# Kernel tuning notes

Hardware: AMD Instinct MI355X
Metric: run time of the kernel (lower is better)

## Reference

```python
import jax, jax.numpy as jnp
import numpy as np

N_ANCHORS = 262144
B = 4
G = 64
IM_SIZE = 1024.0
STRADDLE = 0.0
POS_THR = 0.5
NEG_THR = 0.3
FG_FRAC = 0.3
SAMPLE_BATCH = 512
TARGET_FG = int(FG_FRAC * SAMPLE_BATCH)  # 153
NEG_LOGIT = -1e9


def _jaccard(a, b):
    # Detectron-legacy '+1' box convention. a:[N,4], b:[G,4] -> [N,G]
    area_a = (a[:, 2] - a[:, 0] + 1.0) * (a[:, 3] - a[:, 1] + 1.0)
    area_b = (b[:, 2] - b[:, 0] + 1.0) * (b[:, 3] - b[:, 1] + 1.0)
    lt = jnp.maximum(a[:, None, :2], b[None, :, :2])
    rb = jnp.minimum(a[:, None, 2:], b[None, :, 2:])
    wh = jnp.clip(rb - lt + 1.0, 0.0)
    inter = wh[..., 0] * wh[..., 1]
    return inter / (area_a[:, None] + area_b[None, :] - inter)


def _bbox_transform_inv(ex, gt):
    ew = ex[:, 2] - ex[:, 0] + 1.0
    eh = ex[:, 3] - ex[:, 1] + 1.0
    ecx = ex[:, 0] + 0.5 * ew
    ecy = ex[:, 1] + 0.5 * eh
    gw = gt[:, 2] - gt[:, 0] + 1.0
    gh = gt[:, 3] - gt[:, 1] + 1.0
    gcx = gt[:, 0] + 0.5 * gw
    gcy = gt[:, 1] + 0.5 * gh
    return jnp.stack([(gcx - ecx) / ew, (gcy - ecy) / eh,
                      jnp.log(gw / ew), jnp.log(gh / eh)], axis=1)


def _match_single(boxes, gt_boxes, gt_ignore, im_info, key):
    # mask-based (jit-friendly) equivalent of forward_single_image; outside
    # anchors keep label -1 / targets 0, which reproduces the unmap() step.
    n = boxes.shape[0]
    im_h, im_w = im_info[0], im_info[1]
    inside = ((boxes[:, 0] >= -STRADDLE) & (boxes[:, 1] >= -STRADDLE)
              & (boxes[:, 2] < im_w + STRADDLE + 1.0)
              & (boxes[:, 3] < im_h + STRADDLE + 1.0))
    valid_gt = gt_ignore == 0  # gt_boxes[gt_ignore_labels == 0]
    iou = jnp.where(inside[:, None] & valid_gt[None, :], _jaccard(boxes, gt_boxes), 0.0)
    a2g_max = iou.max(axis=1)
    a2g_idx = iou.argmax(axis=1)
    g2a_max = iou.max(axis=0)
    g2a_max = jnp.where(g2a_max == 0.0, 1.0, g2a_max)  # avoid matching all-zero cols
    with_max = (iou == g2a_max[None, :]).any(axis=1)   # ensure_closest_box
    pos = inside & (with_max | (a2g_max >= POS_THR))
    labels = jnp.where(pos, 1, -1).astype(jnp.int32)
    # subsample positives down to TARGET_FG by random priority (keeps exactly
    # min(fg_num, TARGET_FG) positives, like the permutation-based disable)
    kp, kn = jax.random.split(key)
    prio = jnp.where(pos, jax.random.uniform(kp, (n,)), -jnp.inf)
    rank = jnp.argsort(jnp.argsort(-prio))
    labels = jnp.where(pos & (rank >= TARGET_FG), -1, labels)
    # sample negatives with replacement (torch.multinomial(..., replacement=True))
    num_fg = (labels > 0).sum()
    target_bg = SAMPLE_BATCH - num_fg
    neg = inside & (a2g_max < NEG_THR)
    do_sample = neg.sum() > target_bg
    samp = jax.random.categorical(kn, jnp.where(neg, 0.0, NEG_LOGIT), shape=(SAMPLE_BATCH,))
    valid_s = jnp.arange(SAMPLE_BATCH) < target_bg
    idx = jnp.where(valid_s, samp, n)  # invalid samples write to padded slot
    lab_ext = jnp.concatenate([labels, jnp.full((1,), -1, jnp.int32)])
    lab_samp = lab_ext.at[idx].set(0)[:n]
    labels = jnp.where(do_sample, lab_samp, labels)
    pos_final = labels > 0
    deltas = _bbox_transform_inv(boxes, gt_boxes[a2g_idx])
    bbox_targets = jnp.where(pos_final[:, None], deltas, 0.0)
    return labels, bbox_targets


def setup_inputs() -> dict:
    key = jax.random.key(0)
    k1, k2, k3, k4, k5, k6 = jax.random.split(key, 6)
    axy = jax.random.uniform(k1, (N_ANCHORS, 2), minval=-50.0, maxval=950.0)
    awh = jax.random.uniform(k2, (N_ANCHORS, 2), minval=16.0, maxval=160.0)
    boxes = jnp.concatenate([axy, axy + awh], axis=1)
    gxy = jax.random.uniform(k3, (B, G, 2), minval=0.0, maxval=800.0)
    gwh = jax.random.uniform(k4, (B, G, 2), minval=32.0, maxval=220.0)
    gt_boxes = jnp.concatenate([gxy, gxy + gwh], axis=2)
    gt_labels = jax.random.randint(k5, (B, G), 0, 80)
    gt_ignore_labels = jax.random.randint(k6, (B, G), 0, 2)
    im_info = jnp.tile(jnp.array([IM_SIZE, IM_SIZE, 1.0], jnp.float32), (B, 1))
    return {"boxes": boxes, "gt_boxes": gt_boxes, "gt_labels": gt_labels,
            "gt_ignore_labels": gt_ignore_labels, "im_info": im_info}


def reference(boxes, gt_boxes, gt_labels, gt_ignore_labels, im_info):
    # gt_labels is accepted but unused, exactly as in the torch module
    keys = jax.random.split(jax.random.key(42), gt_boxes.shape[0])
    labels, bbox_targets = jax.vmap(_match_single, in_axes=(None, 0, 0, 0, 0))(
        boxes.reshape(-1, 4), gt_boxes, gt_ignore_labels, im_info, keys)
    return labels, bbox_targets
```

## Files before the change

### kernel.cpp

```cpp
#include <hip/hip_runtime.h>
#include <stdint.h>

#define NANCH   262144
#define NB      4
#define NG      64
#define TGT_FG  153
#define SB      512
#define IDXMASK 262143u
#define NSH     8
#define SHCAP   (NANCH/NSH)

#define WS_PCNT     0
#define WS_KTH      4096
#define WS_TBG      4160
#define WS_DOSAMP   4224
#define WS_NUMPOS   4288
#define WS_G2A      4352
#define WS_SAMPKEY  8192
#define WS_ZERO_BYTES 24576
#define WS_GMAXC    32768
#define WS_A2G      294912
#define WS_NEG      (WS_A2G + NB*NANCH)
#define WS_POS      (WS_NEG + NB*NANCH*4)

#define PCNT_AT(pcnt, b, sh, L) ((pcnt)[(((b) * NSH + (sh)) * 2 + (L)) * 16])

struct RngKeys { uint32_t kp[NB][2]; uint32_t kn[NB][2]; };

#define TFR(r) { x0 += x1; x1 = (x1 << (r)) | (x1 >> (32 - (r))); x1 ^= x0; }
__host__ __device__ inline void tf2x32(uint32_t k0, uint32_t k1,
                                       uint32_t x0, uint32_t x1,
                                       uint32_t &o0, uint32_t &o1) {
  uint32_t k2 = k0 ^ k1 ^ 0x1BD11BDAu;
  x0 += k0; x1 += k1;
  TFR(13) TFR(15) TFR(26) TFR(6)   x0 += k1; x1 += k2 + 1u;
  TFR(17) TFR(29) TFR(16) TFR(24)  x0 += k2; x1 += k0 + 2u;
  TFR(13) TFR(15) TFR(26) TFR(6)   x0 += k0; x1 += k1 + 3u;
  TFR(17) TFR(29) TFR(16) TFR(24)  x0 += k1; x1 += k2 + 4u;
  TFR(13) TFR(15) TFR(26) TFR(6)   x0 += k2; x1 += k0 + 5u;
  o0 = x0; o1 = x1;
}

__host__ __device__ inline void tf_ctr(uint32_t k0, uint32_t k1, uint32_t i,
                                       uint32_t &o0, uint32_t &o1) {
  tf2x32(k0, k1, 0u, i, o0, o1);
}

__device__ __forceinline__ uint32_t draw_bits(uint32_t k0, uint32_t k1,
                                              uint32_t idx) {
  uint32_t o0, o1;
  tf_ctr(k0, k1, idx, o0, o1);
  return o0 ^ o1;
}

#define ROTL1(x, r) __builtin_amdgcn_alignbit((x), (x), 32 - (r))
#define TFQ(r) { x0 += x1; x1 = ROTL1(x1, r); x1 ^= x0; }
__device__ __forceinline__ uint32_t tf_bits_fast(uint32_t k0, uint32_t k1,
                                                 uint32_t k2, uint32_t x0,
                                                 uint32_t x1) {
  TFQ(13) TFQ(15) TFQ(26) TFQ(6)   x0 += k1; x1 += k2 + 1u;
  TFQ(17) TFQ(29) TFQ(16) TFQ(24)  x0 += k2; x1 += k0 + 2u;
  TFQ(13) TFQ(15) TFQ(26) TFQ(6)   x0 += k0; x1 += k1 + 3u;
  TFQ(17) TFQ(29) TFQ(16) TFQ(24)  x0 += k1; x1 += k2 + 4u;
  TFQ(13) TFQ(15) TFQ(26) TFQ(6)   x0 += k2; x1 += k0 + 5u;
  return x0 ^ x1;
}

__device__ __forceinline__ float box_area(float x1, float y1, float x2, float y2) {
#pragma clang fp contract(off)
  return ((x2 - x1) + 1.0f) * ((y2 - y1) + 1.0f);
}

__device__ __forceinline__ float iou_pair(float ax1, float ay1, float ax2, float ay2,
                                          float areaA, float gx1, float gy1,
                                          float gx2, float gy2, float areaB) {
#pragma clang fp contract(off)
  float ltx = fmaxf(ax1, gx1), lty = fmaxf(ay1, gy1);
  float rbx = fminf(ax2, gx2), rby = fminf(ay2, gy2);
  float w = fmaxf((rbx - ltx) + 1.0f, 0.0f);
  float h = fmaxf((rby - lty) + 1.0f, 0.0f);
  float inter = w * h;
  return inter / ((areaA + areaB) - inter);
}

__global__ __launch_bounds__(256) void k_g2amax(
    const float4* __restrict__ boxes, const float4* __restrict__ gtb,
    const int* __restrict__ gti, const float* __restrict__ iminfo,
    float* __restrict__ gmaxc) {
  int bx = blockIdx.x;
  int b = bx >> 8, chunk = bx & 255;
  int t = threadIdx.x, j = t & 63, sub = t >> 6;
  float4 g = gtb[b * NG + j];
  bool valid = (gti[b * NG + j] == 0);
  float areaB = box_area(g.x, g.y, g.z, g.w);
  float thrx = iminfo[b * 3 + 1] + 1.0f;
  float thry = iminfo[b * 3 + 0] + 1.0f;
  float m = 0.0f;
  int base = chunk * 1024 + sub * 256;
  #pragma unroll 2
  for (int i = 0; i < 256; ++i) {
    float4 bb = boxes[base + i];
    bool inside = (bb.x >= -0.0f) && (bb.y >= -0.0f) && (bb.z < thrx) && (bb.w < thry);
    float areaA = box_area(bb.x, bb.y, bb.z, bb.w);
    float v = iou_pair(bb.x, bb.y, bb.z, bb.w, areaA, g.x, g.y, g.z, g.w, areaB);
    v = (inside && valid) ? v : 0.0f;
    m = fmaxf(m, v);
  }
  __shared__ float red[4][64];
  red[sub][j] = m;
  __syncthreads();
  if (t < 64) {
    float mm = fmaxf(fmaxf(red[0][t], red[1][t]), fmaxf(red[2][t], red[3][t]));
    gmaxc[((b << 8) + chunk) * 64 + t] = mm;
  }
}

__global__ __launch_bounds__(256) void k_g2afin(
    const float* __restrict__ gmaxc, float* __restrict__ g2a) {
  int b = blockIdx.x, t = threadIdx.x;
  int j = t & 63, part = t >> 6;
  float m = 0.0f;
  for (int c = part * 64; c < part * 64 + 64; ++c)
    m = fmaxf(m, gmaxc[((b << 8) + c) * 64 + j]);
  __shared__ float red[4][64];
  red[part][j] = m;
  __syncthreads();
  if (t < 64)
    g2a[b * NG + t] = fmaxf(fmaxf(red[0][t], red[1][t]),
                            fmaxf(red[2][t], red[3][t]));
}

__global__ __launch_bounds__(256) void k_label(
    const float4* __restrict__ boxes, const float4* __restrict__ gtb,
    const int* __restrict__ gti, const float* __restrict__ iminfo,
    const float* __restrict__ g2a, float* __restrict__ labels,
    unsigned char* __restrict__ a2g, unsigned long long* __restrict__ pos_keys,
    unsigned int* __restrict__ neg_list, int* __restrict__ pcnt, RngKeys rk) {
  int bx = blockIdx.x;
  int b = bx >> 10, blk = bx & 1023;
  int t = threadIdx.x;
  int sh = blk & (NSH - 1);
  __shared__ float4 sg[NG];
  __shared__ float sab[NG], sval[NG], sadj[NG];
  if (t < NG) {
    float4 g = gtb[b * NG + t];
    sg[t] = g;
    sab[t] = box_area(g.x, g.y, g.z, g.w);
    sval[t] = (gti[b * NG + t] == 0) ? 1.0f : 0.0f;
    float gm = g2a[b * NG + t];
    sadj[t] = (gm == 0.0f) ? 1.0f : gm;
  }
  __syncthreads();
  int a = blk * 256 + t;
  float4 bb = boxes[a];
  float thrx = iminfo[b * 3 + 1] + 1.0f, thry = iminfo[b * 3 + 0] + 1.0f;
  bool inside = (bb.x >= -0.0f) && (bb.y >= -0.0f) && (bb.z < thrx) && (bb.w < thry);
  float areaA = box_area(bb.x, bb.y, bb.z, bb.w);
  float maxv = 0.0f; int amax = 0; bool wm = false;
  #pragma unroll 8
  for (int j = 0; j < NG; ++j) {
    float4 g = sg[j];
    float v = iou_pair(bb.x, bb.y, bb.z, bb.w, areaA, g.x, g.y, g.z, g.w, sab[j]);
    v = (inside && (sval[j] != 0.0f)) ? v : 0.0f;
    wm = wm || (v == sadj[j]);
    if (v > maxv) { maxv = v; amax = j; }
  }
  bool pos = inside && (wm || (maxv >= 0.5f));
  bool neg = inside && (maxv < 0.3f);
  labels[b * NANCH + a] = pos ? 1.0f : -1.0f;
  a2g[b * NANCH + a] = (unsigned char)amax;
  unsigned long long mpos = __ballot(pos);
  unsigned long long mneg = __ballot(neg);
  int lane = t & 63, wid = t >> 6;
  __shared__ int wc[4][2];
  __shared__ int bbase[2];
  if (lane == 0) { wc[wid][0] = __popcll(mpos); wc[wid][1] = __popcll(mneg); }
  __syncthreads();
  if (t == 0) {
    bbase[0] = atomicAdd(&PCNT_AT(pcnt, b, sh, 0),
                         wc[0][0] + wc[1][0] + wc[2][0] + wc[3][0]);
    bbase[1] = atomicAdd(&PCNT_AT(pcnt, b, sh, 1),
                         wc[0][1] + wc[1][1] + wc[2][1] + wc[3][1]);
  }
  __syncthreads();
  unsigned long long lt = (1ull << lane) - 1ull;
  if (pos) {
    int off = bbase[0] + __popcll(mpos & lt);
    for (int w = 0; w < wid; ++w) off += wc[w][0];
    uint32_t bits = draw_bits(rk.kp[b][0], rk.kp[b][1], (uint32_t)a);
    unsigned long long key =
        (((unsigned long long)(bits >> 9)) << 18) | (unsigned long long)(IDXMASK - (uint32_t)a);
    pos_keys[(size_t)b * NANCH + (size_t)sh * SHCAP + off] = key;
  }
  if (neg) {
    int off = bbase[1] + __popcll(mneg & lt);
    for (int w = 0; w < wid; ++w) off += wc[w][1];
    neg_list[(size_t)b * NANCH + (size_t)sh * SHCAP + off] = (unsigned int)a;
  }
}

__global__ __launch_bounds__(256) void k_catsel(
    const unsigned int* __restrict__ neg_list,
    const unsigned long long* __restrict__ pos_keys,
    const int* __restrict__ pcnt, unsigned long long* __restrict__ samp_key,
    unsigned long long* __restrict__ kth, int* __restrict__ tbg,
    int* __restrict__ dosamp, int* __restrict__ numpos, RngKeys rk) {
  int bx = blockIdx.x;
  int t = threadIdx.x, lane = t & 63, wid = t >> 6;

  if (bx < NB) {
    int b = bx;
    __shared__ int cw[4];
    int scnt[NSH]; int np = 0, nnb = 0;
    #pragma unroll
    for (int sh = 0; sh < NSH; ++sh) {
      scnt[sh] = PCNT_AT(pcnt, b, sh, 0);
      np += scnt[sh];
      nnb += PCNT_AT(pcnt, b, sh, 1);
    }
    int nf = np < TGT_FG ? np : TGT_FG;
    int targ = SB - nf;
    if (t == 0) { tbg[b] = targ; dosamp[b] = (nnb > targ) ? 1 : 0; numpos[b] = np; }
    if (np <= TGT_FG) { if (t == 0) kth[b] = 0ull; return; }
    unsigned long long pref = 0ull;
    int r = TGT_FG;
    for (int bit = 40; bit >= 0; --bit) {
      unsigned long long cand = pref | (1ull << bit);
      unsigned long long mask = ~((1ull << bit) - 1ull);
      int c = 0;
      for (int sh = 0; sh < NSH; ++sh) {
        const unsigned long long* keys =
            pos_keys + (size_t)b * NANCH + (size_t)sh * SHCAP;
        for (int i = t; i < scnt[sh]; i += 256)
          c += ((keys[i] & mask) == cand) ? 1 : 0;
      }
      #pragma unroll
      for (int off = 32; off; off >>= 1) c += __shfl_xor(c, off, 64);
      __syncthreads();
      if (lane == 0) cw[wid] = c;
      __syncthreads();
      int total = cw[0] + cw[1] + cw[2] + cw[3];
      if (total >= r) pref = cand; else r -= total;
    }
    if (t == 0) kth[b] = pref;
    return;
  }

  int bx2 = bx - NB;
  int sh = bx2 & (NSH - 1);
  int pr = (bx2 >> 3) & 255;
  int b  = bx2 >> 11;
  int np = 0;
  #pragma unroll
  for (int s = 0; s < NSH; ++s) np += PCNT_AT(pcnt, b, s, 0);
  int targ = SB - (np < TGT_FG ? np : TGT_FG);
  int s0 = pr * 2;
  if (s0 >= targ) return;
  int nn = PCNT_AT(pcnt, b, sh, 1);
  uint32_t k0 = rk.kn[b][0], k1 = rk.kn[b][1];
  uint32_t k2 = k0 ^ k1 ^ 0x1BD11BDAu;
  uint32_t xb0 = ((uint32_t)s0 << 18) + k1;
  uint32_t xb1 = ((uint32_t)(s0 + 1) << 18) + k1;
  unsigned long long b0 = 0ull, b1 = 0ull;
  const unsigned int* nl = neg_list + (size_t)b * NANCH + (size_t)sh * SHCAP;
#define PROC1(A) { uint32_t a_ = (A); \
    unsigned long long inv64 = (unsigned long long)(IDXMASK - a_); \
    { uint32_t bits = tf_bits_fast(k0, k1, k2, k0, xb0 + a_); \
      unsigned long long key = (((unsigned long long)(bits >> 9)) << 18) | inv64; \
      if (key > b0) b0 = key; } \
    { uint32_t bits = tf_bits_fast(k0, k1, k2, k0, xb1 + a_); \
      unsigned long long key = (((unsigned long long)(bits >> 9)) << 18) | inv64; \
      if (key > b1) b1 = key; } }
  int nv = nn >> 2;
  const uint4* nl4 = (const uint4*)nl;
  for (int iv = t; iv < nv; iv += 256) {
    uint4 q = nl4[iv];
    PROC1(q.x) PROC1(q.y) PROC1(q.z) PROC1(q.w)
  }
  for (int i = (nv << 2) + t; i < nn; i += 256) { PROC1(nl[i]) }
#undef PROC1
  #pragma unroll
  for (int off = 32; off; off >>= 1) {
    unsigned long long o0 = __shfl_xor(b0, off, 64); if (o0 > b0) b0 = o0;
    unsigned long long o1 = __shfl_xor(b1, off, 64); if (o1 > b1) b1 = o1;
  }
  __shared__ unsigned long long red[4][2];
  if (lane == 0) { red[wid][0] = b0; red[wid][1] = b1; }
  __syncthreads();
  if (t < 2) {
    int j = t;
    unsigned long long m = red[0][j];
    if (red[1][j] > m) m = red[1][j];
    if (red[2][j] > m) m = red[2][j];
    if (red[3][j] > m) m = red[3][j];
    if (s0 + j < targ) atomicMax(&samp_key[b * SB + s0 + j], m);
  }
}

__global__ __launch_bounds__(256) void k_disable(
    const unsigned long long* __restrict__ pos_keys, const int* __restrict__ pcnt,
    const int* __restrict__ numpos, const unsigned long long* __restrict__ kth,
    float* __restrict__ labels) {
  int b = blockIdx.x >> 6, blk = blockIdx.x & 63;
  if (numpos[b] <= TGT_FG) return;
  int sh = blk & (NSH - 1), sub = blk >> 3;
  int cnt = PCNT_AT(pcnt, b, sh, 0);
  unsigned long long K = kth[b];
  const unsigned long long* keys = pos_keys + (size_t)b * NANCH + (size_t)sh * SHCAP;
  for (int i = sub * 256 + threadIdx.x; i < cnt; i += 8 * 256) {
    unsigned long long key = keys[i];
    if (key < K) {
      int a = (int)(IDXMASK - (uint32_t)(key & (unsigned long long)IDXMASK));
      labels[b * NANCH + a] = -1.0f;
    }
  }
}

__global__ __launch_bounds__(256) void k_scatter(
    const unsigned long long* __restrict__ samp_key, const int* __restrict__ tbg,
    const int* __restrict__ dosamp, float* __restrict__ labels) {
  int b = blockIdx.x >> 1;
  int s = ((blockIdx.x & 1) << 8) | threadIdx.x;
  if (!dosamp[b]) return;
  if (s < tbg[b]) {
    unsigned long long key = samp_key[b * SB + s];
    int a = (int)(IDXMASK - (uint32_t)(key & (unsigned long long)IDXMASK));
    labels[b * NANCH + a] = 0.0f;
  }
}

__global__ __launch_bounds__(256) void k_targets(
    const float4* __restrict__ boxes, const float4* __restrict__ gtb,
    const unsigned char* __restrict__ a2g, const float* __restrict__ labels,
    float4* __restrict__ tout) {
  int bx = blockIdx.x;
  int b = bx >> 10, blk = bx & 1023;
  int a = blk * 256 + threadIdx.x;
  float lab = labels[b * NANCH + a];
  float4 o = make_float4(0.f, 0.f, 0.f, 0.f);
  if (lab > 0.0f) {
    float4 e = boxes[a];
    float4 g = gtb[b * NG + a2g[b * NANCH + a]];
    float ew = e.z - e.x + 1.0f, eh = e.w - e.y + 1.0f;
    float ecx = e.x + 0.5f * ew, ecy = e.y + 0.5f * eh;
    float gw = g.z - g.x + 1.0f, gh = g.w - g.y + 1.0f;
    float gcx = g.x + 0.5f * gw, gcy = g.y + 0.5f * gh;
    o.x = (gcx - ecx) / ew;
    o.y = (gcy - ecy) / eh;
    o.z = logf(gw / ew);
    o.w = logf(gh / eh);
  }
  tout[(size_t)b * NANCH + a] = o;
}

extern "C" void kernel_launch(void* const* d_in, const int* in_sizes, int n_in,
                              void* d_out, int out_size, void* d_ws, size_t ws_size,
                              hipStream_t stream) {
  const float4* boxes  = (const float4*)d_in[0];
  const float4* gtb    = (const float4*)d_in[1];
  const int*    gti    = (const int*)d_in[3];
  const float*  iminfo = (const float*)d_in[4];
  float*  labels = (float*)d_out;
  float4* tout   = (float4*)(labels + (size_t)NB * NANCH);

  char* wsb = (char*)d_ws;
  int*                pcnt     = (int*)(wsb + WS_PCNT);
  unsigned long long* kth      = (unsigned long long*)(wsb + WS_KTH);
  int*                tbg      = (int*)(wsb + WS_TBG);
  int*                dosamp   = (int*)(wsb + WS_DOSAMP);
  int*                numpos   = (int*)(wsb + WS_NUMPOS);
  float*              g2a_f    = (float*)(wsb + WS_G2A);
  unsigned long long* samp_key = (unsigned long long*)(wsb + WS_SAMPKEY);
  float*              gmaxc    = (float*)(wsb + WS_GMAXC);
  unsigned char*      a2g      = (unsigned char*)(wsb + WS_A2G);
  unsigned int*       neg_list = (unsigned int*)(wsb + WS_NEG);
  unsigned long long* pos_keys = (unsigned long long*)(wsb + WS_POS);

  RngKeys rk;
  for (int b = 0; b < NB; ++b) {
    uint32_t a0, a1;
    tf_ctr(0u, 42u, (uint32_t)b, a0, a1);
    tf_ctr(a0, a1, 0u, rk.kp[b][0], rk.kp[b][1]);
    tf_ctr(a0, a1, 1u, rk.kn[b][0], rk.kn[b][1]);
  }

  hipMemsetAsync(wsb, 0, WS_ZERO_BYTES, stream);
  k_g2amax <<<NB * (NANCH / 1024), 256, 0, stream>>>(boxes, gtb, gti, iminfo, gmaxc);
  k_g2afin <<<NB, 256, 0, stream>>>(gmaxc, g2a_f);
  k_label  <<<NB * (NANCH / 256), 256, 0, stream>>>(boxes, gtb, gti, iminfo, g2a_f,
                                                    labels, a2g, pos_keys, neg_list,
                                                    pcnt, rk);
  k_catsel <<<NB + NB * 256 * NSH, 256, 0, stream>>>(neg_list, pos_keys, pcnt,
                                                     samp_key, kth, tbg, dosamp,
                                                     numpos, rk);
  k_disable<<<NB * 64, 256, 0, stream>>>(pos_keys, pcnt, numpos, kth, labels);
  k_scatter<<<NB * 2, 256, 0, stream>>>(samp_key, tbg, dosamp, labels);
  k_targets<<<NB * (NANCH / 256), 256, 0, stream>>>(boxes, gtb, a2g, labels, tout);
}
```

Measured before the change: 745.7 us.

## Fuse memset, g2a finalize and positive-disable into neighbouring kernels

Drops the workspace memset by having block 0 of k_g2amax zero it. Drops k_g2afin by having every k_label block redo the per-GT max reduction over the chunk maxima. Drops k_disable by having k_targets recompute each positive's random key and compare it against the k-th threshold. The aim is to remove three launches and their dependency gaps. The cost is that every one of the 4096 k_label blocks now reads the full 64 KB gmaxc slice for its batch, which adds heavy redundant L2 traffic, and k_targets does extra Threefry work for positive anchors.

```diff
diff --git a/kernel.cpp b/kernel.cpp
--- a/kernel.cpp
+++ b/kernel.cpp
@@ -14,10 +14,8 @@
 #define WS_KTH      4096
 #define WS_TBG      4160
 #define WS_DOSAMP   4224
-#define WS_NUMPOS   4288
-#define WS_G2A      4352
 #define WS_SAMPKEY  8192
-#define WS_ZERO_BYTES 24576
+#define WS_ZERO_WORDS 6144
 #define WS_GMAXC    32768
 #define WS_A2G      294912
 #define WS_NEG      (WS_A2G + NB*NANCH)
@@ -86,10 +84,15 @@
 __global__ __launch_bounds__(256) void k_g2amax(
     const float4* __restrict__ boxes, const float4* __restrict__ gtb,
     const int* __restrict__ gti, const float* __restrict__ iminfo,
-    float* __restrict__ gmaxc) {
+    float* __restrict__ gmaxc, unsigned int* __restrict__ wszero) {
   int bx = blockIdx.x;
+  int t = threadIdx.x;
+  if (bx == 0) {
+    #pragma unroll
+    for (int i = t; i < WS_ZERO_WORDS; i += 256) wszero[i] = 0u;
+  }
   int b = bx >> 8, chunk = bx & 255;
-  int t = threadIdx.x, j = t & 63, sub = t >> 6;
+  int j = t & 63, sub = t >> 6;
   float4 g = gtb[b * NG + j];
   bool valid = (gti[b * NG + j] == 0);
   float areaB = box_area(g.x, g.y, g.z, g.w);
@@ -115,25 +118,10 @@
   }
 }
 
-__global__ __launch_bounds__(256) void k_g2afin(
-    const float* __restrict__ gmaxc, float* __restrict__ g2a) {
-  int b = blockIdx.x, t = threadIdx.x;
-  int j = t & 63, part = t >> 6;
-  float m = 0.0f;
-  for (int c = part * 64; c < part * 64 + 64; ++c)
-    m = fmaxf(m, gmaxc[((b << 8) + c) * 64 + j]);
-  __shared__ float red[4][64];
-  red[part][j] = m;
-  __syncthreads();
-  if (t < 64)
-    g2a[b * NG + t] = fmaxf(fmaxf(red[0][t], red[1][t]),
-                            fmaxf(red[2][t], red[3][t]));
-}
-
 __global__ __launch_bounds__(256) void k_label(
     const float4* __restrict__ boxes, const float4* __restrict__ gtb,
     const int* __restrict__ gti, const float* __restrict__ iminfo,
-    const float* __restrict__ g2a, float* __restrict__ labels,
+    const float* __restrict__ gmaxc, float* __restrict__ labels,
     unsigned char* __restrict__ a2g, unsigned long long* __restrict__ pos_keys,
     unsigned int* __restrict__ neg_list, int* __restrict__ pcnt, RngKeys rk) {
   int bx = blockIdx.x;
@@ -142,12 +130,23 @@
   int sh = blk & (NSH - 1);
   __shared__ float4 sg[NG];
   __shared__ float sab[NG], sval[NG], sadj[NG];
+  __shared__ float red2[4][64];
+  {
+    int j = t & 63, part = t >> 6;
+    float m = 0.0f;
+    for (int c = part * 64; c < part * 64 + 64; ++c)
+      m = fmaxf(m, gmaxc[((b << 8) + c) * 64 + j]);
+    red2[part][j] = m;
+  }
   if (t < NG) {
     float4 g = gtb[b * NG + t];
     sg[t] = g;
     sab[t] = box_area(g.x, g.y, g.z, g.w);
     sval[t] = (gti[b * NG + t] == 0) ? 1.0f : 0.0f;
-    float gm = g2a[b * NG + t];
+  }
+  __syncthreads();
+  if (t < 64) {
+    float gm = fmaxf(fmaxf(red2[0][t], red2[1][t]), fmaxf(red2[2][t], red2[3][t]));
     sadj[t] = (gm == 0.0f) ? 1.0f : gm;
   }
   __syncthreads();
@@ -204,7 +203,7 @@
     const unsigned long long* __restrict__ pos_keys,
     const int* __restrict__ pcnt, unsigned long long* __restrict__ samp_key,
     unsigned long long* __restrict__ kth, int* __restrict__ tbg,
-    int* __restrict__ dosamp, int* __restrict__ numpos, RngKeys rk) {
+    int* __restrict__ dosamp, RngKeys rk) {
   int bx = blockIdx.x;
   int t = threadIdx.x, lane = t & 63, wid = t >> 6;
 
@@ -220,7 +219,7 @@
     }
     int nf = np < TGT_FG ? np : TGT_FG;
     int targ = SB - nf;
-    if (t == 0) { tbg[b] = targ; dosamp[b] = (nnb > targ) ? 1 : 0; numpos[b] = np; }
+    if (t == 0) { tbg[b] = targ; dosamp[b] = (nnb > targ) ? 1 : 0; }
     if (np <= TGT_FG) { if (t == 0) kth[b] = 0ull; return; }
     unsigned long long pref = 0ull;
     int r = TGT_FG;
@@ -297,25 +296,6 @@
   }
 }
 
-__global__ __launch_bounds__(256) void k_disable(
-    const unsigned long long* __restrict__ pos_keys, const int* __restrict__ pcnt,
-    const int* __restrict__ numpos, const unsigned long long* __restrict__ kth,
-    float* __restrict__ labels) {
-  int b = blockIdx.x >> 6, blk = blockIdx.x & 63;
-  if (numpos[b] <= TGT_FG) return;
-  int sh = blk & (NSH - 1), sub = blk >> 3;
-  int cnt = PCNT_AT(pcnt, b, sh, 0);
-  unsigned long long K = kth[b];
-  const unsigned long long* keys = pos_keys + (size_t)b * NANCH + (size_t)sh * SHCAP;
-  for (int i = sub * 256 + threadIdx.x; i < cnt; i += 8 * 256) {
-    unsigned long long key = keys[i];
-    if (key < K) {
-      int a = (int)(IDXMASK - (uint32_t)(key & (unsigned long long)IDXMASK));
-      labels[b * NANCH + a] = -1.0f;
-    }
-  }
-}
-
 __global__ __launch_bounds__(256) void k_scatter(
     const unsigned long long* __restrict__ samp_key, const int* __restrict__ tbg,
     const int* __restrict__ dosamp, float* __restrict__ labels) {
@@ -331,24 +311,32 @@
 
 __global__ __launch_bounds__(256) void k_targets(
     const float4* __restrict__ boxes, const float4* __restrict__ gtb,
-    const unsigned char* __restrict__ a2g, const float* __restrict__ labels,
-    float4* __restrict__ tout) {
+    const unsigned char* __restrict__ a2g, float* __restrict__ labels,
+    const unsigned long long* __restrict__ kth, float4* __restrict__ tout,
+    RngKeys rk) {
   int bx = blockIdx.x;
   int b = bx >> 10, blk = bx & 1023;
   int a = blk * 256 + threadIdx.x;
   float lab = labels[b * NANCH + a];
   float4 o = make_float4(0.f, 0.f, 0.f, 0.f);
   if (lab > 0.0f) {
-    float4 e = boxes[a];
-    float4 g = gtb[b * NG + a2g[b * NANCH + a]];
-    float ew = e.z - e.x + 1.0f, eh = e.w - e.y + 1.0f;
-    float ecx = e.x + 0.5f * ew, ecy = e.y + 0.5f * eh;
-    float gw = g.z - g.x + 1.0f, gh = g.w - g.y + 1.0f;
-    float gcx = g.x + 0.5f * gw, gcy = g.y + 0.5f * gh;
-    o.x = (gcx - ecx) / ew;
-    o.y = (gcy - ecy) / eh;
-    o.z = logf(gw / ew);
-    o.w = logf(gh / eh);
+    uint32_t bits = draw_bits(rk.kp[b][0], rk.kp[b][1], (uint32_t)a);
+    unsigned long long key =
+        (((unsigned long long)(bits >> 9)) << 18) | (unsigned long long)(IDXMASK - (uint32_t)a);
+    if (key < kth[b]) {
+      labels[b * NANCH + a] = -1.0f;
+    } else {
+      float4 e = boxes[a];
+      float4 g = gtb[b * NG + a2g[b * NANCH + a]];
+      float ew = e.z - e.x + 1.0f, eh = e.w - e.y + 1.0f;
+      float ecx = e.x + 0.5f * ew, ecy = e.y + 0.5f * eh;
+      float gw = g.z - g.x + 1.0f, gh = g.w - g.y + 1.0f;
+      float gcx = g.x + 0.5f * gw, gcy = g.y + 0.5f * gh;
+      o.x = (gcx - ecx) / ew;
+      o.y = (gcy - ecy) / eh;
+      o.z = logf(gw / ew);
+      o.w = logf(gh / eh);
+    }
   }
   tout[(size_t)b * NANCH + a] = o;
 }
@@ -368,8 +356,6 @@
   unsigned long long* kth      = (unsigned long long*)(wsb + WS_KTH);
   int*                tbg      = (int*)(wsb + WS_TBG);
   int*                dosamp   = (int*)(wsb + WS_DOSAMP);
-  int*                numpos   = (int*)(wsb + WS_NUMPOS);
-  float*              g2a_f    = (float*)(wsb + WS_G2A);
   unsigned long long* samp_key = (unsigned long long*)(wsb + WS_SAMPKEY);
   float*              gmaxc    = (float*)(wsb + WS_GMAXC);
   unsigned char*      a2g      = (unsigned char*)(wsb + WS_A2G);
@@ -384,16 +370,14 @@
     tf_ctr(a0, a1, 1u, rk.kn[b][0], rk.kn[b][1]);
   }
 
-  hipMemsetAsync(wsb, 0, WS_ZERO_BYTES, stream);
-  k_g2amax <<<NB * (NANCH / 1024), 256, 0, stream>>>(boxes, gtb, gti, iminfo, gmaxc);
-  k_g2afin <<<NB, 256, 0, stream>>>(gmaxc, g2a_f);
-  k_label  <<<NB * (NANCH / 256), 256, 0, stream>>>(boxes, gtb, gti, iminfo, g2a_f,
+  k_g2amax <<<NB * (NANCH / 1024), 256, 0, stream>>>(boxes, gtb, gti, iminfo,
+                                                     gmaxc, (unsigned int*)wsb);
+  k_label  <<<NB * (NANCH / 256), 256, 0, stream>>>(boxes, gtb, gti, iminfo, gmaxc,
                                                     labels, a2g, pos_keys, neg_list,
                                                     pcnt, rk);
   k_catsel <<<NB + NB * 256 * NSH, 256, 0, stream>>>(neg_list, pos_keys, pcnt,
-                                                     samp_key, kth, tbg, dosamp,
-                                                     numpos, rk);
-  k_disable<<<NB * 64, 256, 0, stream>>>(pos_keys, pcnt, numpos, kth, labels);
+                                                     samp_key, kth, tbg, dosamp, rk);
   k_scatter<<<NB * 2, 256, 0, stream>>>(samp_key, tbg, dosamp, labels);
-  k_targets<<<NB * (NANCH / 256), 256, 0, stream>>>(boxes, gtb, a2g, labels, tout);
-}
+  k_targets<<<NB * (NANCH / 256), 256, 0, stream>>>(boxes, gtb, a2g, labels,
+                                                    kth, tout, rk);
+}
```

Measured after the change: 749.9 us. Within noise of the previous version (+0.6%).
